# Optimization experiments

Hardware: AMD Instinct MI355X
Metric: run time of the kernel (lower is better)

## Reference

```python
import jax, jax.numpy as jnp
import numpy as np

IM_SIZE = (384, 384)
GRID_OVERSAMP = 1.25
GRID_SIZE = tuple(round(s * GRID_OVERSAMP) for s in IM_SIZE)  # (480, 480)
N, C, K = 1, 16, 500000


def setup_inputs() -> dict:
    key = jax.random.key(0)
    k1, k2, k3 = jax.random.split(key, 3)
    img_real = jax.random.normal(k1, (N, C) + IM_SIZE, dtype=jnp.float32)
    img_imag = jax.random.normal(k2, (N, C) + IM_SIZE, dtype=jnp.float32)
    # continuous k-space trajectory coords in [-s/2, s/2) per dim
    u = jax.random.uniform(k3, (N, K, 2), dtype=jnp.float32)
    trj = (u - 0.5) * jnp.asarray(IM_SIZE, dtype=jnp.float32)
    return {"img_real": img_real, "img_imag": img_imag, "trj": trj}


def _rescale_trajectory(trj):
    # trj * oversamp, shift to [0, gs-1], round -> int32 grid indices
    gs = jnp.asarray(GRID_SIZE, dtype=jnp.float32)
    trj_rs = trj * GRID_OVERSAMP
    trj_rs = jnp.clip(trj_rs + gs / 2, 0.0, gs - 1)
    return jnp.round(trj_rs).astype(jnp.int32)


def _forward_complex(img, idx):
    # PadLast: center-pad last d dims from im_size to grid size
    pads = [((g - s) // 2, g - s - (g - s) // 2) for g, s in zip(GRID_SIZE, IM_SIZE)]
    img_os = jnp.pad(img, ((0, 0), (0, 0), pads[0], pads[1]))
    # sp_fft: centered orthonormal FFT over spatial dims
    axes = (-2, -1)
    ksp_os = jnp.fft.fftshift(
        jnp.fft.fftn(jnp.fft.ifftshift(img_os, axes=axes), axes=axes, norm="ortho"),
        axes=axes,
    )  # (N, C, Gx, Gy) complex64
    # per-batch irregular gather at rounded grid indices (multi_index)
    gather = jax.vmap(lambda k, t: k[:, t[:, 0], t[:, 1]])(ksp_os, idx)  # (N, C, K)
    return gather


def reference(img_real, img_imag, trj):
    img = (img_real + 1j * img_imag).astype(jnp.complex64)
    idx = _rescale_trajectory(trj)
    ksp = _forward_complex(img, idx)
    # return real/imag stacked so output is a float tensor: (2, N, C, K)
    return jnp.stack([ksp.real, ksp.imag]).astype(jnp.float32)
```

## Files before the change

### kernel.cpp

```cpp
#include <hip/hip_runtime.h>
#include <math.h>

#define PI_F 3.14159265358979323846f
#define LSTRIDE 488

__device__ __forceinline__ void dft2(float* vr, float* vi) {
  float ar = vr[0], ai = vi[0];
  vr[0] = ar + vr[1]; vi[0] = ai + vi[1];
  vr[1] = ar - vr[1]; vi[1] = ai - vi[1];
}

__device__ __forceinline__ void dft3(float* vr, float* vi) {
  const float s3 = 0.86602540378443864676f;
  float t1r = vr[1] + vr[2], t1i = vi[1] + vi[2];
  float t2r = vr[1] - vr[2], t2i = vi[1] - vi[2];
  float ar = vr[0] - 0.5f * t1r, ai = vi[0] - 0.5f * t1i;
  float br = s3 * t2r, bi = s3 * t2i;
  vr[0] = vr[0] + t1r; vi[0] = vi[0] + t1i;
  vr[1] = ar + bi; vi[1] = ai - br;
  vr[2] = ar - bi; vi[2] = ai + br;
}

__device__ __forceinline__ void dft4(float* vr, float* vi) {
  float t0r = vr[0] + vr[2], t0i = vi[0] + vi[2];
  float t1r = vr[0] - vr[2], t1i = vi[0] - vi[2];
  float t2r = vr[1] + vr[3], t2i = vi[1] + vi[3];
  float t3r = vr[1] - vr[3], t3i = vi[1] - vi[3];
  vr[0] = t0r + t2r; vi[0] = t0i + t2i;
  vr[2] = t0r - t2r; vi[2] = t0i - t2i;
  vr[1] = t1r + t3i; vi[1] = t1i - t3r;
  vr[3] = t1r - t3i; vi[3] = t1i + t3r;
}

__device__ __forceinline__ void dft5(float* vr, float* vi) {
  const float c1 = 0.30901699437494742410f, s1 = 0.95105651629515357212f;
  const float c2 = -0.80901699437494742410f, s2 = 0.58778525229247312917f;
  float t1r = vr[1] + vr[4], t1i = vi[1] + vi[4];
  float t2r = vr[2] + vr[3], t2i = vi[2] + vi[3];
  float t3r = vr[1] - vr[4], t3i = vi[1] - vi[4];
  float t4r = vr[2] - vr[3], t4i = vi[2] - vi[3];
  float a1r = vr[0] + c1 * t1r + c2 * t2r, a1i = vi[0] + c1 * t1i + c2 * t2i;
  float a2r = vr[0] + c2 * t1r + c1 * t2r, a2i = vi[0] + c2 * t1i + c1 * t2i;
  float b1r = s1 * t3r + s2 * t4r, b1i = s1 * t3i + s2 * t4i;
  float b2r = s2 * t3r - s1 * t4r, b2i = s2 * t3i - s1 * t4i;
  vr[0] = vr[0] + t1r + t2r; vi[0] = vi[0] + t1i + t2i;
  vr[1] = a1r + b1i; vi[1] = a1i - b1r;
  vr[4] = a1r - b1i; vi[4] = a1i + b1r;
  vr[2] = a2r + b2i; vi[2] = a2i - b2r;
  vr[3] = a2r - b2i; vi[3] = a2i + b2r;
}

template <int R, int Ls>
__device__ __forceinline__ void fft_stage(const float* sre, const float* sim,
                                          float* dre, float* dim_, int lane) {
  const int M = 480 / R;
  const float w = -2.0f * PI_F / (float)(Ls * R);
  for (int i = lane; i < M; i += 64) {
    const int j = i % Ls, k = i / Ls;
    float vr[R], vi[R];
#pragma unroll
    for (int r = 0; r < R; ++r) { vr[r] = sre[i + r * M]; vi[r] = sim[i + r * M]; }
    if constexpr (Ls > 1) {
#pragma unroll
      for (int r = 1; r < R; ++r) {
        float s, c;
        __sincosf(w * (float)(j * r), &s, &c);
        float tr = vr[r] * c - vi[r] * s;
        vi[r] = vr[r] * s + vi[r] * c;
        vr[r] = tr;
      }
    }
    if constexpr (R == 2) dft2(vr, vi);
    else if constexpr (R == 3) dft3(vr, vi);
    else if constexpr (R == 4) dft4(vr, vi);
    else dft5(vr, vi);
    const int base = k * (Ls * R) + j;
#pragma unroll
    for (int r = 0; r < R; ++r) { dre[base + r * Ls] = vr[r]; dim_[base + r * Ls] = vi[r]; }
  }
}

__device__ __forceinline__ void fft480(float* reA, float* imA, float* reB, float* imB,
                                       int lane) {
  fft_stage<5, 1>(reA, imA, reB, imB, lane);   __syncthreads();
  fft_stage<4, 5>(reB, imB, reA, imA, lane);   __syncthreads();
  fft_stage<4, 20>(reA, imA, reB, imB, lane);  __syncthreads();
  fft_stage<3, 80>(reB, imB, reA, imA, lane);  __syncthreads();
  fft_stage<2, 240>(reA, imA, reB, imB, lane); __syncthreads();
}

__global__ __launch_bounds__(512) void pass1_kernel(const float* __restrict__ imgr,
                                                    const float* __restrict__ imgi,
                                                    float2* __restrict__ A) {
  __shared__ float sA[2][8][LSTRIDE];
  __shared__ float sB[2][8][LSTRIDE];
  const int lb = threadIdx.x >> 6, lane = threadIdx.x & 63;
  const int g0 = blockIdx.x * 8;
  const int c = g0 / 384, x0 = g0 % 384;
  const int xp = x0 + lb;
  const float* rowr = imgr + (size_t)(c * 384 + xp) * 384;
  const float* rowi = imgi + (size_t)(c * 384 + xp) * 384;
  float* reA = &sA[0][lb][0]; float* imA = &sA[1][lb][0];
  float* reB = &sB[0][lb][0]; float* imB = &sB[1][lb][0];

  for (int y = lane; y < 480; y += 64) {
    float r = 0.f, im = 0.f;
    if (y >= 48 && y < 432) {
      const int yp = y - 48;
      const float sgn = ((xp + yp) & 1) ? -1.f : 1.f;
      r = rowr[yp] * sgn; im = rowi[yp] * sgn;
    }
    reA[y] = r; imA[y] = im;
  }
  __syncthreads();
  fft480(reA, imA, reB, imB, lane);
  for (int e = threadIdx.x; e < 480 * 8; e += 512) {
    const int v = e >> 3, xb = e & 7;
    A[((size_t)(c * 480 + v)) * 384 + (x0 + xb)] = make_float2(sB[0][xb][v], sB[1][xb][v]);
  }
}

__global__ __launch_bounds__(512) void pass2_kernel(const float2* __restrict__ A,
                                                    float2* __restrict__ B) {
  __shared__ float sA[2][8][LSTRIDE];
  __shared__ float sB[2][8][LSTRIDE];
  const int lb = threadIdx.x >> 6, lane = threadIdx.x & 63;
  const int v = blockIdx.x >> 1, half = blockIdx.x & 1;
  const int c = half * 8 + lb;
  const float2* Arow = A + ((size_t)(c * 480 + v)) * 384;
  float* reA = &sA[0][lb][0]; float* imA = &sA[1][lb][0];
  float* reB = &sB[0][lb][0]; float* imB = &sB[1][lb][0];

  for (int x = lane; x < 480; x += 64) {
    float r = 0.f, im = 0.f;
    if (x >= 48 && x < 432) { float2 t = Arow[x - 48]; r = t.x; im = t.y; }
    reA[x] = r; imA[x] = im;
  }
  __syncthreads();
  fft480(reA, imA, reB, imB, lane);
  const float inv = 1.0f / 480.0f;
  for (int e = threadIdx.x; e < 480 * 8; e += 512) {
    const int u = e >> 3, w2 = e & 7;
    B[((size_t)v * 480 + u) * 16 + half * 8 + w2] =
        make_float2(sB[0][w2][u] * inv, sB[1][w2][u] * inv);
  }
}

__global__ __launch_bounds__(256) void gather_kernel(const float2* __restrict__ B,
                                                     const float* __restrict__ trj,
                                                     float* __restrict__ out) {
  const int k = blockIdx.x * 256 + threadIdx.x;
  if (k >= 500000) return;
  const float2 t = ((const float2*)trj)[k];
  float p0 = t.x * 1.25f;
  float p1 = t.y * 1.25f;
  asm volatile("" : "+v"(p0), "+v"(p1));
  float v0 = p0 + 240.0f;
  float v1 = p1 + 240.0f;
  v0 = fminf(fmaxf(v0, 0.0f), 479.0f);
  v1 = fminf(fmaxf(v1, 0.0f), 479.0f);
  const int i0 = (int)rintf(v0);
  const int i1 = (int)rintf(v1);
  const float scale = ((i0 + i1) & 1) ? -1.0f : 1.0f;
  const float4* cell = (const float4*)(B + ((size_t)i1 * 480 + i0) * 16);
#pragma unroll
  for (int cc = 0; cc < 8; ++cc) {
    float4 q = cell[cc];
    const int c = 2 * cc;
    __builtin_nontemporal_store(q.x * scale, &out[(size_t)c * 500000 + k]);
    __builtin_nontemporal_store(q.y * scale, &out[8000000 + (size_t)c * 500000 + k]);
    __builtin_nontemporal_store(q.z * scale, &out[(size_t)(c + 1) * 500000 + k]);
    __builtin_nontemporal_store(q.w * scale, &out[8000000 + (size_t)(c + 1) * 500000 + k]);
  }
}

extern "C" void kernel_launch(void* const* d_in, const int* in_sizes, int n_in,
                              void* d_out, int out_size, void* d_ws, size_t ws_size,
                              hipStream_t stream) {
  const float* imgr = (const float*)d_in[0];
  const float* imgi = (const float*)d_in[1];
  const float* trj  = (const float*)d_in[2];
  float* out = (float*)d_out;

  const size_t A_floats = (size_t)16 * 384 * 480 * 2;
  float2* A = (float2*)(out + (16000000 - A_floats));
  float2* B = (float2*)d_ws;

  hipLaunchKernelGGL(pass1_kernel, dim3(16 * 384 / 8), dim3(512), 0, stream, imgr, imgi, A);
  hipLaunchKernelGGL(pass2_kernel, dim3(480 * 2), dim3(512), 0, stream, A, B);
  hipLaunchKernelGGL(gather_kernel, dim3((500000 + 255) / 256), dim3(256), 0, stream,
                     B, trj, out);
}
```

Baseline: 133.1 us.

## Use radix-8 FFT stage and wave-level barriers within per-wave FFT rows

The 480-point FFT is refactored from five stages (5,4,4,3,2) to four (5,8,4,3) by adding a radix-8 butterfly, which cuts one LDS round trip and one set of twiddle computations per row. Because each wavefront owns its own row, the inter-stage block-wide __syncthreads are replaced by wave barriers with a compiler memory fence, leaving a single block barrier before the transposed write-out. The result now ends in the A buffers, so the output reads are redirected to match. Correctness relies on LDS ordering within a wave being guaranteed by the wave barrier.

```diff
diff --git a/kernel.cpp b/kernel.cpp
--- a/kernel.cpp
+++ b/kernel.cpp
@@ -3,6 +3,11 @@
 
 #define PI_F 3.14159265358979323846f
 #define LSTRIDE 488
+
+__device__ __forceinline__ void wave_sync() {
+  __builtin_amdgcn_wave_barrier();
+  asm volatile("" ::: "memory");
+}
 
 __device__ __forceinline__ void dft2(float* vr, float* vi) {
   float ar = vr[0], ai = vi[0];
@@ -50,6 +55,26 @@
   vr[3] = a2r - b2i; vi[3] = a2i + b2r;
 }
 
+__device__ __forceinline__ void dft8(float* vr, float* vi) {
+  float er[4]  = {vr[0], vr[2], vr[4], vr[6]};
+  float ei[4]  = {vi[0], vi[2], vi[4], vi[6]};
+  float or_[4] = {vr[1], vr[3], vr[5], vr[7]};
+  float oi[4]  = {vi[1], vi[3], vi[5], vi[7]};
+  dft4(er, ei); dft4(or_, oi);
+  const float h = 0.70710678118654752440f;
+  float t1r = h * (or_[1] + oi[1]), t1i = h * (oi[1] - or_[1]);
+  float t2r = oi[2],                t2i = -or_[2];
+  float t3r = h * (oi[3] - or_[3]), t3i = -h * (or_[3] + oi[3]);
+  vr[0] = er[0] + or_[0]; vi[0] = ei[0] + oi[0];
+  vr[4] = er[0] - or_[0]; vi[4] = ei[0] - oi[0];
+  vr[1] = er[1] + t1r;    vi[1] = ei[1] + t1i;
+  vr[5] = er[1] - t1r;    vi[5] = ei[1] - t1i;
+  vr[2] = er[2] + t2r;    vi[2] = ei[2] + t2i;
+  vr[6] = er[2] - t2r;    vi[6] = ei[2] - t2i;
+  vr[3] = er[3] + t3r;    vi[3] = ei[3] + t3i;
+  vr[7] = er[3] - t3r;    vi[7] = ei[3] - t3i;
+}
+
 template <int R, int Ls>
 __device__ __forceinline__ void fft_stage(const float* sre, const float* sim,
                                           float* dre, float* dim_, int lane) {
@@ -73,7 +98,8 @@
     if constexpr (R == 2) dft2(vr, vi);
     else if constexpr (R == 3) dft3(vr, vi);
     else if constexpr (R == 4) dft4(vr, vi);
-    else dft5(vr, vi);
+    else if constexpr (R == 5) dft5(vr, vi);
+    else dft8(vr, vi);
     const int base = k * (Ls * R) + j;
 #pragma unroll
     for (int r = 0; r < R; ++r) { dre[base + r * Ls] = vr[r]; dim_[base + r * Ls] = vi[r]; }
@@ -82,11 +108,10 @@
 
 __device__ __forceinline__ void fft480(float* reA, float* imA, float* reB, float* imB,
                                        int lane) {
-  fft_stage<5, 1>(reA, imA, reB, imB, lane);   __syncthreads();
-  fft_stage<4, 5>(reB, imB, reA, imA, lane);   __syncthreads();
-  fft_stage<4, 20>(reA, imA, reB, imB, lane);  __syncthreads();
-  fft_stage<3, 80>(reB, imB, reA, imA, lane);  __syncthreads();
-  fft_stage<2, 240>(reA, imA, reB, imB, lane); __syncthreads();
+  fft_stage<5, 1>(reA, imA, reB, imB, lane);    wave_sync();
+  fft_stage<8, 5>(reB, imB, reA, imA, lane);    wave_sync();
+  fft_stage<4, 40>(reA, imA, reB, imB, lane);   wave_sync();
+  fft_stage<3, 160>(reB, imB, reA, imA, lane);
 }
 
 __global__ __launch_bounds__(512) void pass1_kernel(const float* __restrict__ imgr,
@@ -112,11 +137,12 @@
     }
     reA[y] = r; imA[y] = im;
   }
+  wave_sync();
+  fft480(reA, imA, reB, imB, lane);
   __syncthreads();
-  fft480(reA, imA, reB, imB, lane);
   for (int e = threadIdx.x; e < 480 * 8; e += 512) {
     const int v = e >> 3, xb = e & 7;
-    A[((size_t)(c * 480 + v)) * 384 + (x0 + xb)] = make_float2(sB[0][xb][v], sB[1][xb][v]);
+    A[((size_t)(c * 480 + v)) * 384 + (x0 + xb)] = make_float2(sA[0][xb][v], sA[1][xb][v]);
   }
 }
 
@@ -136,13 +162,14 @@
     if (x >= 48 && x < 432) { float2 t = Arow[x - 48]; r = t.x; im = t.y; }
     reA[x] = r; imA[x] = im;
   }
+  wave_sync();
+  fft480(reA, imA, reB, imB, lane);
   __syncthreads();
-  fft480(reA, imA, reB, imB, lane);
   const float inv = 1.0f / 480.0f;
   for (int e = threadIdx.x; e < 480 * 8; e += 512) {
     const int u = e >> 3, w2 = e & 7;
     B[((size_t)v * 480 + u) * 16 + half * 8 + w2] =
-        make_float2(sB[0][w2][u] * inv, sB[1][w2][u] * inv);
+        make_float2(sA[0][w2][u] * inv, sA[1][w2][u] * inv);
   }
 }
 
```

Result: faster. 126.8 us (-4.8%).
